# Optimization experiments

Measured on AMD Instinct MI355X. Metric: run time of the kernel, lower is better.

Reference implementation:

```python
import jax, jax.numpy as jnp
import numpy as np

B, S, E, H, DH = 4, 2048, 2048, 16, 256  # DH = mlp hidden (d_hid)
HD = E // H  # per-head dim = 128
EPS = 1e-5

def _ln(x, w, b):
    m = jnp.mean(x, axis=-1, keepdims=True)
    v = jnp.mean(jnp.square(x - m), axis=-1, keepdims=True)
    return (x - m) * jax.lax.rsqrt(v + EPS) * w + b

def setup_inputs() -> dict:
    key = jax.random.key(0)
    ks = jax.random.split(key, 10)
    s = 0.02
    return {
        "x": jax.random.normal(ks[0], (B, S, E), jnp.float32),
        "attention_mask": jax.random.randint(ks[1], (B, S), 0, 2, jnp.int32),
        "ln1_w": jnp.ones((E,), jnp.float32),
        "ln1_b": jnp.zeros((E,), jnp.float32),
        "in_proj_w": jax.random.normal(ks[2], (3 * E, E), jnp.float32) * s,
        "in_proj_b": jnp.zeros((3 * E,), jnp.float32),
        "out_proj_w": jax.random.normal(ks[3], (E, E), jnp.float32) * s,
        "out_proj_b": jnp.zeros((E,), jnp.float32),
        "ln2_w": jnp.ones((E,), jnp.float32),
        "ln2_b": jnp.zeros((E,), jnp.float32),
        "mlp_w1": jax.random.normal(ks[4], (DH, E), jnp.float32) * s,
        "mlp_b1": jnp.zeros((DH,), jnp.float32),
        "mlp_w2": jax.random.normal(ks[5], (E, DH), jnp.float32) * s,
        "mlp_b2": jnp.zeros((E,), jnp.float32),
    }

def reference(x, attention_mask, ln1_w, ln1_b, in_proj_w, in_proj_b,
              out_proj_w, out_proj_b, ln2_w, ln2_b, mlp_w1, mlp_b1, mlp_w2, mlp_b2):
    h = _ln(x, ln1_w, ln1_b)
    qkv = h @ in_proj_w.T + in_proj_b  # [B,S,3E]
    q, k, v = jnp.split(qkv, 3, axis=-1)
    q = q.reshape(B, S, H, HD).transpose(0, 2, 1, 3) / jnp.sqrt(jnp.float32(HD))
    k = k.reshape(B, S, H, HD).transpose(0, 2, 1, 3)
    v = v.reshape(B, S, H, HD).transpose(0, 2, 1, 3)
    scores = jnp.einsum("bhqd,bhkd->bhqk", q, k)
    # Faithful to source: FLOAT attn_mask of +1.0 on strictly-upper triangle (additive),
    # NOT -inf; key_padding_mask positions do get -inf.
    causal_add = jnp.triu(jnp.ones((S, S), jnp.float32), k=1)
    scores = scores + causal_add
    pad = (attention_mask == 0)  # True = padded key
    scores = jnp.where(pad[:, None, None, :], jnp.float32(-jnp.inf), scores)
    attn = jax.nn.softmax(scores, axis=-1)
    ctx = jnp.einsum("bhqk,bhkd->bhqd", attn, v)
    ctx = ctx.transpose(0, 2, 1, 3).reshape(B, S, E)
    x = x + ctx @ out_proj_w.T + out_proj_b
    h2 = _ln(x, ln2_w, ln2_b)
    mlp = jax.nn.relu(h2 @ mlp_w1.T + mlp_b1) @ mlp_w2.T + mlp_b2
    return x + mlp
```

## Files before the change

### kernel.cpp

```cpp
#include <hip/hip_runtime.h>

typedef __attribute__((ext_vector_type(8))) short short8;
typedef __attribute__((ext_vector_type(4))) float f32x4;
typedef __attribute__((ext_vector_type(16))) float f32x16;

typedef __attribute__((address_space(1))) const void gas1_t;
typedef __attribute__((address_space(3))) void las3_t;
#define GLL16(g, l) __builtin_amdgcn_global_load_lds((gas1_t*)(g), (las3_t*)(l), 16, 0, 0)

__device__ inline unsigned short f2bf(float f) {
  union { float f; unsigned int u; } v; v.f = f;
  unsigned int r = v.u + 0x7FFFu + ((v.u >> 16) & 1u);
  return (unsigned short)(r >> 16);
}

__device__ inline float exp2_fast(float x) {
  float r; asm("v_exp_f32 %0, %1" : "=v"(r) : "v"(x)); return r;
}

__device__ inline void vmwait(int n) {
  if (n == 6)      asm volatile("s_waitcnt vmcnt(6)" ::: "memory");
  else             asm volatile("s_waitcnt vmcnt(0)" ::: "memory");
}

__global__ __launch_bounds__(256) void ln_kernel(const float* __restrict__ x,
                                                 const float* __restrict__ w,
                                                 const float* __restrict__ bia,
                                                 unsigned short* __restrict__ out) {
  const int row = blockIdx.x;
  const int tid = threadIdx.x;
  const float* xr = x + (size_t)row * 2048;
  float4 a = *(const float4*)(xr + tid * 8);
  float4 b = *(const float4*)(xr + tid * 8 + 4);
  float s  = a.x + a.y + a.z + a.w + b.x + b.y + b.z + b.w;
  float s2 = a.x*a.x + a.y*a.y + a.z*a.z + a.w*a.w + b.x*b.x + b.y*b.y + b.z*b.z + b.w*b.w;
  #pragma unroll
  for (int off = 1; off < 64; off <<= 1) {
    s  += __shfl_xor(s, off);
    s2 += __shfl_xor(s2, off);
  }
  __shared__ float red[8];
  if ((tid & 63) == 0) { red[tid >> 6] = s; red[4 + (tid >> 6)] = s2; }
  __syncthreads();
  s  = red[0] + red[1] + red[2] + red[3];
  s2 = red[4] + red[5] + red[6] + red[7];
  const float mean = s * (1.f / 2048.f);
  const float var  = s2 * (1.f / 2048.f) - mean * mean;
  const float rstd = rsqrtf(var + 1e-5f);
  float4 wa = *(const float4*)(w + tid * 8), wb = *(const float4*)(w + tid * 8 + 4);
  float4 ba = *(const float4*)(bia + tid * 8), bb = *(const float4*)(bia + tid * 8 + 4);
  short8 o;
  o[0] = (short)f2bf((a.x - mean) * rstd * wa.x + ba.x);
  o[1] = (short)f2bf((a.y - mean) * rstd * wa.y + ba.y);
  o[2] = (short)f2bf((a.z - mean) * rstd * wa.z + ba.z);
  o[3] = (short)f2bf((a.w - mean) * rstd * wa.w + ba.w);
  o[4] = (short)f2bf((b.x - mean) * rstd * wb.x + bb.x);
  o[5] = (short)f2bf((b.y - mean) * rstd * wb.y + bb.y);
  o[6] = (short)f2bf((b.z - mean) * rstd * wb.z + bb.z);
  o[7] = (short)f2bf((b.w - mean) * rstd * wb.w + bb.w);
  *(short8*)(out + (size_t)row * 2048 + tid * 8) = o;
}

__global__ __launch_bounds__(256) void conv_kernel(const float* __restrict__ in,
                                                   unsigned short* __restrict__ out, int n) {
  size_t idx = ((size_t)blockIdx.x * 256 + threadIdx.x) * 8;
  if (idx >= (size_t)n) return;
  float4 a = *(const float4*)(in + idx);
  float4 b = *(const float4*)(in + idx + 4);
  short8 o;
  o[0] = (short)f2bf(a.x); o[1] = (short)f2bf(a.y);
  o[2] = (short)f2bf(a.z); o[3] = (short)f2bf(a.w);
  o[4] = (short)f2bf(b.x); o[5] = (short)f2bf(b.y);
  o[6] = (short)f2bf(b.z); o[7] = (short)f2bf(b.w);
  *(short8*)(out + idx) = o;
}

template <int MODE>
__global__ __launch_bounds__(256) void gemm_bt(const unsigned short* __restrict__ A,
                                               const unsigned short* __restrict__ Bw,
                                               const float* __restrict__ bias,
                                               const float* __restrict__ res,
                                               void* __restrict__ outp,
                                               void* __restrict__ outp2,
                                               int M, int N, int K) {
  __shared__ unsigned short As[128 * 64];
  __shared__ unsigned short Bs[128 * 64];
  const int tid = threadIdx.x;
  const int l = tid & 63, wv = tid >> 6;
  const int l15 = l & 15, l4 = l >> 4;
  const int wr = wv >> 1, wc = wv & 1;
  const int nx = gridDim.x;
  const int nwg = nx * gridDim.y;
  const int bidlin = blockIdx.y * nx + blockIdx.x;
  const int cpx = nwg >> 3;
  const int swz = (bidlin & 7) * cpx + (bidlin >> 3);
  const int m0 = (swz / nx) * 128, n0 = (swz % nx) * 128;

  f32x4 acc[4][4] = {};
  for (int k0 = 0; k0 < K; k0 += 64) {
    __syncthreads();
    #pragma unroll
    for (int i = 0; i < 4; ++i) {
      int e = i * 2048 + tid * 8;
      int r = e >> 6;
      int c = (e ^ ((r & 7) << 3)) & 63;
      GLL16(A + (size_t)(m0 + r) * K + k0 + c, As + e);
      GLL16(Bw + (size_t)(n0 + r) * K + k0 + c, Bs + e);
    }
    __syncthreads();
    #pragma unroll
    for (int kk = 0; kk < 64; kk += 32) {
      short8 af[4], bfr[4];
      #pragma unroll
      for (int m = 0; m < 4; ++m) {
        int r = wr * 64 + m * 16 + l15;
        int byt = (r * 128 + (kk + l4 * 8) * 2) ^ ((r & 7) << 4);
        af[m] = *(const short8*)((const char*)As + byt);
      }
      #pragma unroll
      for (int n = 0; n < 4; ++n) {
        int r = wc * 64 + n * 16 + l15;
        int byt = (r * 128 + (kk + l4 * 8) * 2) ^ ((r & 7) << 4);
        bfr[n] = *(const short8*)((const char*)Bs + byt);
      }
      #pragma unroll
      for (int m = 0; m < 4; ++m)
        #pragma unroll
        for (int n = 0; n < 4; ++n)
          acc[m][n] = __builtin_amdgcn_mfma_f32_16x16x32_bf16(af[m], bfr[n], acc[m][n], 0, 0, 0);
    }
  }
  #pragma unroll
  for (int m = 0; m < 4; ++m) {
    #pragma unroll
    for (int n = 0; n < 4; ++n) {
      #pragma unroll
      for (int r = 0; r < 4; ++r) {
        int row = m0 + wr * 64 + m * 16 + l4 * 4 + r;
        int col = n0 + wc * 64 + n * 16 + l15;
        float v = acc[m][n][r] + bias[col];
        if (MODE == 1) {
          ((unsigned short*)outp)[(size_t)row * N + col] = f2bf(v > 0.f ? v : 0.f);
        } else {
          ((float*)outp)[(size_t)row * N + col] = res[(size_t)row * N + col] + v;
        }
      }
    }
  }
}

template <int MODE>
__global__ __launch_bounds__(512, 2) void gemm8(const unsigned short* __restrict__ A,
                                                const unsigned short* __restrict__ Bw,
                                                const float* __restrict__ bias,
                                                const float* __restrict__ res,
                                                void* __restrict__ outp,
                                                int M, int N, int K) {
  __shared__ char LA[2][2][16384];
  __shared__ char LB[2][2][16384];
  const int tid = threadIdx.x;
  const int l = tid & 63, wv = tid >> 6;
  const int l15 = l & 15, l4 = l >> 4;
  const int wr = wv >> 2, wc = wv & 3;
  const int wch = wc >> 1, wcl = wc & 1;
  const int nx = gridDim.x;
  const int nwg = nx * gridDim.y;
  const int bidlin = blockIdx.y * nx + blockIdx.x;
  const int cpx = nwg >> 3;
  const int swz = (bidlin & 7) * cpx + (bidlin >> 3);
  const int m0 = (swz / nx) * 256, n0 = (swz % nx) * 256;

  const int srow = tid >> 3;
  const int scol = ((tid & 7) ^ (srow & 7)) * 8;

#define STG_A(x, h) { const unsigned short* bp = A + (size_t)(m0 + (h) * 128) * K + (x) * 64; \
    GLL16(bp + (size_t)srow * K + scol, &LA[(x) & 1][h][tid * 16]); \
    GLL16(bp + (size_t)(srow + 64) * K + scol, &LA[(x) & 1][h][8192 + tid * 16]); }
#define STG_B(x, h) { const unsigned short* bp = Bw + (size_t)(n0 + (h) * 128) * K + (x) * 64; \
    GLL16(bp + (size_t)srow * K + scol, &LB[(x) & 1][h][tid * 16]); \
    GLL16(bp + (size_t)(srow + 64) * K + scol, &LB[(x) & 1][h][8192 + tid * 16]); }

#define FOFF(r, kh) ((r) * 128 + (((((kh) * 4 + l4)) ^ ((r) & 7)) << 4))

  f32x4 acc[8][4] = {};
  const int NT = K >> 6;

  STG_A(0, 0); STG_A(0, 1); STG_B(0, 0); STG_B(0, 1);
  STG_B(1, 0); STG_B(1, 1); STG_A(1, 0);
  vmwait(6);
  __builtin_amdgcn_s_barrier();

#define MFMAK(mh, kh) \
    __builtin_amdgcn_s_setprio(1); \
    _Pragma("unroll") for (int f = 0; f < 4; ++f) \
      _Pragma("unroll") for (int n = 0; n < 4; ++n) { \
        if (MODE == 3) \
          acc[(mh) * 4 + f][n] = __builtin_amdgcn_mfma_f32_16x16x32_bf16( \
              bfr[kh][n], af[kh][f], acc[(mh) * 4 + f][n], 0, 0, 0); \
        else \
          acc[(mh) * 4 + f][n] = __builtin_amdgcn_mfma_f32_16x16x32_bf16( \
              af[kh][f], bfr[kh][n], acc[(mh) * 4 + f][n], 0, 0, 0); \
      } \
    __builtin_amdgcn_s_setprio(0);

  for (int t = 0; t < NT; ++t) {
    const char* Ab = LA[t & 1][wr];
    const char* Bb = LB[t & 1][wch];
    short8 af[2][4], bfr[2][4];
    #pragma unroll
    for (int f = 0; f < 4; ++f) {
      bfr[0][f] = *(const short8*)(Bb + FOFF(wcl * 64 + f * 16 + l15, 0));
      af[0][f]  = *(const short8*)(Ab + FOFF(f * 16 + l15, 0));
    }
    __builtin_amdgcn_sched_barrier(0);
    #pragma unroll
    for (int f = 0; f < 4; ++f) {
      bfr[1][f] = *(const short8*)(Bb + FOFF(wcl * 64 + f * 16 + l15, 1));
      af[1][f]  = *(const short8*)(Ab + FOFF(f * 16 + l15, 1));
    }
    if (t + 1 < NT) STG_A(t + 1, 1);
    __builtin_amdgcn_s_barrier();
    asm volatile("s_waitcnt lgkmcnt(8)" ::: "memory");
    __builtin_amdgcn_sched_barrier(0);
    MFMAK(0, 0);
    asm volatile("s_waitcnt lgkmcnt(0)" ::: "memory");
    __builtin_amdgcn_sched_barrier(0);
    MFMAK(0, 1);
    __builtin_amdgcn_s_barrier();
    #pragma unroll
    for (int f = 0; f < 4; ++f)
      af[0][f] = *(const short8*)(Ab + FOFF(64 + f * 16 + l15, 0));
    __builtin_amdgcn_sched_barrier(0);
    #pragma unroll
    for (int f = 0; f < 4; ++f)
      af[1][f] = *(const short8*)(Ab + FOFF(64 + f * 16 + l15, 1));
    if (t + 2 < NT) { STG_B(t + 2, 0); STG_B(t + 2, 1); STG_A(t + 2, 0); }
    __builtin_amdgcn_s_barrier();
    asm volatile("s_waitcnt lgkmcnt(4)" ::: "memory");
    __builtin_amdgcn_sched_barrier(0);
    MFMAK(1, 0);
    asm volatile("s_waitcnt lgkmcnt(0)" ::: "memory");
    __builtin_amdgcn_sched_barrier(0);
    MFMAK(1, 1);
    vmwait(t >= NT - 2 ? 0 : 6);
    __builtin_amdgcn_s_barrier();
  }
#undef MFMAK
#undef FOFF
#undef STG_A
#undef STG_B

  #pragma unroll
  for (int mf = 0; mf < 8; ++mf) {
    #pragma unroll
    for (int nf = 0; nf < 4; ++nf) {
      #pragma unroll
      for (int r = 0; r < 4; ++r) {
        if (MODE == 3) {
          int vcol = n0 + wc * 64 + nf * 16 + l4 * 4 + r;
          int token = m0 + wr * 128 + mf * 16 + l15;
          float v = acc[mf][nf][r] + bias[vcol];
          int hh = vcol >> 7, d = vcol & 127;
          int bb = token >> 11;
          ((unsigned short*)outp)[((size_t)(bb * 16 + hh) * 128 + d) * 2048 +
                                  (token & 2047)] = f2bf(v);
        } else {
          int row = m0 + wr * 128 + mf * 16 + l4 * 4 + r;
          int col = n0 + wc * 64 + nf * 16 + l15;
          float v = acc[mf][nf][r] + bias[col];
          if (MODE == 0) {
            ((unsigned short*)outp)[(size_t)row * 4096 + col] = f2bf(v);
          } else {
            ((float*)outp)[(size_t)row * N + col] = res[(size_t)row * N + col] + v;
          }
        }
      }
    }
  }
}

__global__ __launch_bounds__(256) void attn_kernel(const unsigned short* __restrict__ qk,
                                                   const unsigned short* __restrict__ vT,
                                                   const int* __restrict__ amask,
                                                   unsigned short* __restrict__ ctx) {
  __shared__ unsigned short Ks[2][4096];
  __shared__ unsigned short Vs[2][4096];

  const int lin = blockIdx.y * 16 + blockIdx.x;
  const int swzb = (lin & 7) * 128 + (lin >> 3);
  const int qt = swzb & 15, bh = swzb >> 4;
  const int b = bh >> 4, h = bh & 15;
  const int tid = threadIdx.x;
  const int wv = tid >> 6, l = tid & 63;
  const int l31 = l & 31, hi = l >> 5;
  const int q0w = qt * 128 + wv * 32;
  const float SC2 = 0.08838834764831845f * 1.4426950408889634f;
  const float L2E = 1.4426950408889634f;
  const float MF  = 10.0f;

  int kinv[2], vinv[2];
  #pragma unroll
  for (int c = 0; c < 2; ++c) {
    int e = c * 2048 + tid * 8;
    int key = e >> 7, d0 = e & 127;
    kinv[c] = key * 4096 + 2048 + h * 128 + (d0 ^ ((key & 7) << 3));
    int d = e >> 5, kchunk = ((e >> 3) & 3) ^ ((d & 6) >> 1);
    vinv[c] = d * 2048 + kchunk * 8;
  }
  const unsigned short* kb0 = qk + (size_t)(b * 2048) * 4096;
  const unsigned short* vb0 = vT + (size_t)(b * 16 + h) * (128 * 2048);
  const int* mrow = amask + b * 2048;

  short8 qf[8];
  {
    const unsigned short* qp = qk + (size_t)(b * 2048 + q0w + l31) * 4096 + h * 128 + hi * 8;
    #pragma unroll
    for (int c = 0; c < 8; ++c) qf[c] = *(const short8*)(qp + c * 16);
  }

  short8 vones;
  #pragma unroll
  for (int j = 0; j < 8; ++j) vones[j] = (short)0x3F80;

  f32x16 o[4] = {};
  f32x16 ol = {};

  #pragma unroll
  for (int c = 0; c < 2; ++c) {
    GLL16(kb0 + kinv[c], &Ks[0][c * 2048 + tid * 8]);
    GLL16(vb0 + vinv[c], &Vs[0][c * 2048 + tid * 8]);
  }
  __syncthreads();

  for (int kt = 0; kt < 2048; kt += 32) {
    const int cur = (kt >> 5) & 1;
    if (kt + 32 < 2048) {
      #pragma unroll
      for (int c = 0; c < 2; ++c) {
        GLL16(kb0 + (size_t)(kt + 32) * 4096 + kinv[c], &Ks[cur ^ 1][c * 2048 + tid * 8]);
        GLL16(vb0 + (kt + 32) + vinv[c], &Vs[cur ^ 1][c * 2048 + tid * 8]);
      }
    }
    const unsigned bm = (unsigned)__ballot((l < 32) && (mrow[kt + l31] == 0));
    const unsigned bmh = bm >> (4 * hi);

    f32x16 sacc = {};
    __builtin_amdgcn_s_setprio(1);
    #pragma unroll
    for (int c = 0; c < 8; ++c) {
      short8 kf = *(const short8*)((const char*)Ks[cur] +
                   ((l31 * 256 + c * 32 + hi * 16) ^ ((l31 & 7) << 4)));
      sacc = __builtin_amdgcn_mfma_f32_32x32x16_bf16(kf, qf[c], sacc, 0, 0, 0);
    }
    __builtin_amdgcn_s_setprio(0);

    const int Dq = q0w + l31 - kt - 4 * hi;
    float p[16];
    if (kt > q0w + 31) {
      #pragma unroll
      for (int i = 0; i < 16; ++i) p[i] = sacc[i] * SC2 + (L2E - MF);
    } else if (kt + 31 <= q0w) {
      #pragma unroll
      for (int i = 0; i < 16; ++i) p[i] = sacc[i] * SC2 - MF;
    } else {
      #pragma unroll
      for (int i = 0; i < 16; ++i) {
        const int ci = (i & 3) + 8 * (i >> 2);
        p[i] = sacc[i] * SC2 + ((ci > Dq) ? (L2E - MF) : -MF);
      }
    }
    #pragma unroll
    for (int i = 0; i < 16; ++i) {
      const int ci = (i & 3) + 8 * (i >> 2);
      if ((bmh >> ci) & 1) p[i] = -1e30f;
    }
    #pragma unroll
    for (int i = 0; i < 16; ++i) p[i] = exp2_fast(p[i]);

#define CVTPK(dst, a, bsrc) asm("v_cvt_pk_bf16_f32 %0, %1, %2" : "=v"(dst) : "v"(a), "v"(bsrc))
#define PLSWAP(fst, snd) asm("v_permlane32_swap_b32 %0, %1" : "+v"(fst), "+v"(snd))
    unsigned x, x2, y, y2, u, u2, v, v2;
    CVTPK(x,  p[0],  p[1]);  CVTPK(x2, p[2],  p[3]);
    CVTPK(y,  p[4],  p[5]);  CVTPK(y2, p[6],  p[7]);
    CVTPK(u,  p[8],  p[9]);  CVTPK(u2, p[10], p[11]);
    CVTPK(v,  p[12], p[13]); CVTPK(v2, p[14], p[15]);
    PLSWAP(x, y);  PLSWAP(x2, y2);
    PLSWAP(u, v);  PLSWAP(u2, v2);
    union { unsigned w[4]; short8 s8; } P0, P1;
    P0.w[0] = x; P0.w[1] = x2; P0.w[2] = y; P0.w[3] = y2;
    P1.w[0] = u; P1.w[1] = u2; P1.w[2] = v; P1.w[3] = v2;
    short8 pa0 = P0.s8, pa1 = P1.s8;
#undef CVTPK
#undef PLSWAP

    __builtin_amdgcn_s_setprio(1);
    #pragma unroll
    for (int g = 0; g < 4; ++g) {
      int d = g * 32 + l31;
      int swzd = (d & 6) << 3;
      short8 vf0 = *(const short8*)((const char*)Vs[cur] + ((d * 64 + hi * 16) ^ swzd));
      o[g] = __builtin_amdgcn_mfma_f32_32x32x16_bf16(pa0, vf0, o[g], 0, 0, 0);
      short8 vf1 = *(const short8*)((const char*)Vs[cur] + ((d * 64 + 32 + hi * 16) ^ swzd));
      o[g] = __builtin_amdgcn_mfma_f32_32x32x16_bf16(pa1, vf1, o[g], 0, 0, 0);
    }
    ol = __builtin_amdgcn_mfma_f32_32x32x16_bf16(pa0, vones, ol, 0, 0, 0);
    ol = __builtin_amdgcn_mfma_f32_32x32x16_bf16(pa1, vones, ol, 0, 0, 0);
    __builtin_amdgcn_s_setprio(0);

    __syncthreads();
  }

  float inv[16];
  #pragma unroll
  for (int i = 0; i < 16; ++i) inv[i] = 1.0f / ol[i];
  #pragma unroll
  for (int g = 0; g < 4; ++g) {
    #pragma unroll
    for (int i = 0; i < 16; ++i) {
      int q = q0w + (i & 3) + 8 * (i >> 2) + 4 * hi;
      ctx[(size_t)(b * 2048 + q) * 2048 + h * 128 + g * 32 + l31] = f2bf(o[g][i] * inv[i]);
    }
  }
}

extern "C" void kernel_launch(void* const* d_in, const int* in_sizes, int n_in,
                              void* d_out, int out_size, void* d_ws, size_t ws_size,
                              hipStream_t stream) {
  (void)in_sizes; (void)n_in; (void)out_size; (void)ws_size;
  const float* x    = (const float*)d_in[0];
  const int*   am   = (const int*)d_in[1];
  const float* ln1w = (const float*)d_in[2];
  const float* ln1b = (const float*)d_in[3];
  const float* win  = (const float*)d_in[4];
  const float* bin  = (const float*)d_in[5];
  const float* wout = (const float*)d_in[6];
  const float* bout = (const float*)d_in[7];
  const float* ln2w = (const float*)d_in[8];
  const float* ln2b = (const float*)d_in[9];
  const float* w1   = (const float*)d_in[10];
  const float* b1   = (const float*)d_in[11];
  const float* w2   = (const float*)d_in[12];
  const float* b2   = (const float*)d_in[13];
  float* out = (float*)d_out;

  char* ws = (char*)d_ws;
  unsigned short* hbuf = (unsigned short*)ws;
  unsigned short* ctxb = (unsigned short*)ws;
  unsigned short* qkb  = (unsigned short*)(ws + (size_t)32 * 1048576);
  unsigned short* h2b  = (unsigned short*)(ws + (size_t)32 * 1048576);
  unsigned short* midb = (unsigned short*)(ws + (size_t)64 * 1048576);
  unsigned short* vTb  = (unsigned short*)(ws + (size_t)96 * 1048576);
  unsigned short* wbuf = (unsigned short*)(ws + (size_t)128 * 1048576);

  ln_kernel<<<dim3(8192), dim3(256), 0, stream>>>(x, ln1w, ln1b, hbuf);
  conv_kernel<<<dim3(6144), dim3(256), 0, stream>>>(win, wbuf, 12582912);
  gemm8<0><<<dim3(16, 32), dim3(512), 0, stream>>>(hbuf, wbuf, bin, (const float*)nullptr,
                                                   (void*)qkb, 8192, 4096, 2048);
  gemm8<3><<<dim3(8, 32), dim3(512), 0, stream>>>(hbuf, wbuf + (size_t)4096 * 2048,
                                                  bin + 4096, (const float*)nullptr,
                                                  (void*)vTb, 8192, 2048, 2048);
  attn_kernel<<<dim3(16, 64), dim3(256), 0, stream>>>(qkb, vTb, am, ctxb);
  conv_kernel<<<dim3(2048), dim3(256), 0, stream>>>(wout, wbuf, 4194304);
  gemm8<2><<<dim3(8, 32), dim3(512), 0, stream>>>(ctxb, wbuf, bout, x,
                                                  (void*)out, 8192, 2048, 2048);
  ln_kernel<<<dim3(8192), dim3(256), 0, stream>>>(out, ln2w, ln2b, h2b);
  conv_kernel<<<dim3(256), dim3(256), 0, stream>>>(w1, wbuf, 524288);
  gemm_bt<1><<<dim3(2, 64), dim3(256), 0, stream>>>(h2b, wbuf, b1, (const float*)nullptr,
                                                    (void*)midb, nullptr, 8192, 256, 2048);
  conv_kernel<<<dim3(256), dim3(256), 0, stream>>>(w2, wbuf, 524288);
  gemm8<2><<<dim3(8, 32), dim3(512), 0, stream>>>(midb, wbuf, b2, out,
                                                  (void*)out, 8192, 2048, 256);
}
```

Measured before the change: 592.4 us.

## Fold key padding mask into V projection and row-sum MFMA operand

Removes the per-tile ballot on the attention mask and the per-element masking of softmax probabilities. Padded keys are handled instead by zeroing their V rows in the V-projection epilogue and by using a 0/1 mask vector (staged in LDS) as the row-sum MFMA operand, so masked keys contribute nothing to numerator or denominator. This takes global mask loads and select instructions out of the attention inner loop, at the cost of a mask read in the GEMM epilogue and two small LDS reads per tile. It relies on the fixed max offset making exp finite for masked scores; an all-padded row would still divide by zero, which the reference would also yield as NaN.

Result: no change. 584.3 us (-1.4%).

```diff
diff --git a/kernel.cpp b/kernel.cpp
--- a/kernel.cpp
+++ b/kernel.cpp
@@ -154,6 +154,7 @@
                                                 const unsigned short* __restrict__ Bw,
                                                 const float* __restrict__ bias,
                                                 const float* __restrict__ res,
+                                                const int* __restrict__ amask,
                                                 void* __restrict__ outp,
                                                 int M, int N, int K) {
   __shared__ char LA[2][2][16384];
@@ -252,18 +253,22 @@
 
   #pragma unroll
   for (int mf = 0; mf < 8; ++mf) {
+    int tokenv = 0, amv = 1;
+    if (MODE == 3) {
+      tokenv = m0 + wr * 128 + mf * 16 + l15;
+      amv = amask[tokenv];
+    }
     #pragma unroll
     for (int nf = 0; nf < 4; ++nf) {
       #pragma unroll
       for (int r = 0; r < 4; ++r) {
         if (MODE == 3) {
           int vcol = n0 + wc * 64 + nf * 16 + l4 * 4 + r;
-          int token = m0 + wr * 128 + mf * 16 + l15;
-          float v = acc[mf][nf][r] + bias[vcol];
+          float v = (amv != 0) ? (acc[mf][nf][r] + bias[vcol]) : 0.f;
           int hh = vcol >> 7, d = vcol & 127;
-          int bb = token >> 11;
+          int bb = tokenv >> 11;
           ((unsigned short*)outp)[((size_t)(bb * 16 + hh) * 128 + d) * 2048 +
-                                  (token & 2047)] = f2bf(v);
+                                  (tokenv & 2047)] = f2bf(v);
         } else {
           int row = m0 + wr * 128 + mf * 16 + l4 * 4 + r;
           int col = n0 + wc * 64 + nf * 16 + l15;
@@ -285,6 +290,7 @@
                                                    unsigned short* __restrict__ ctx) {
   __shared__ unsigned short Ks[2][4096];
   __shared__ unsigned short Vs[2][4096];
+  __shared__ unsigned short validbf[2048];
 
   const int lin = blockIdx.y * 16 + blockIdx.x;
   const int swzb = (lin & 7) * 128 + (lin >> 3);
@@ -311,6 +317,14 @@
   const unsigned short* vb0 = vT + (size_t)(b * 16 + h) * (128 * 2048);
   const int* mrow = amask + b * 2048;
 
+  {
+    int i8 = tid * 8;
+    short8 vv;
+    #pragma unroll
+    for (int j = 0; j < 8; ++j) vv[j] = (short)(mrow[i8 + j] ? 0x3F80 : 0);
+    *(short8*)&validbf[i8] = vv;
+  }
+
   short8 qf[8];
   {
     const unsigned short* qp = qk + (size_t)(b * 2048 + q0w + l31) * 4096 + h * 128 + hi * 8;
@@ -318,10 +332,6 @@
     for (int c = 0; c < 8; ++c) qf[c] = *(const short8*)(qp + c * 16);
   }
 
-  short8 vones;
-  #pragma unroll
-  for (int j = 0; j < 8; ++j) vones[j] = (short)0x3F80;
-
   f32x16 o[4] = {};
   f32x16 ol = {};
 
@@ -341,8 +351,6 @@
         GLL16(vb0 + (kt + 32) + vinv[c], &Vs[cur ^ 1][c * 2048 + tid * 8]);
       }
     }
-    const unsigned bm = (unsigned)__ballot((l < 32) && (mrow[kt + l31] == 0));
-    const unsigned bmh = bm >> (4 * hi);
 
     f32x16 sacc = {};
     __builtin_amdgcn_s_setprio(1);
@@ -368,11 +376,6 @@
         const int ci = (i & 3) + 8 * (i >> 2);
         p[i] = sacc[i] * SC2 + ((ci > Dq) ? (L2E - MF) : -MF);
       }
-    }
-    #pragma unroll
-    for (int i = 0; i < 16; ++i) {
-      const int ci = (i & 3) + 8 * (i >> 2);
-      if ((bmh >> ci) & 1) p[i] = -1e30f;
     }
     #pragma unroll
     for (int i = 0; i < 16; ++i) p[i] = exp2_fast(p[i]);
@@ -393,6 +396,9 @@
 #undef CVTPK
 #undef PLSWAP
 
+    short8 vm0 = *(const short8*)&validbf[kt + hi * 8];
+    short8 vm1 = *(const short8*)&validbf[kt + 16 + hi * 8];
+
     __builtin_amdgcn_s_setprio(1);
     #pragma unroll
     for (int g = 0; g < 4; ++g) {
@@ -403,8 +409,8 @@
       short8 vf1 = *(const short8*)((const char*)Vs[cur] + ((d * 64 + 32 + hi * 16) ^ swzd));
       o[g] = __builtin_amdgcn_mfma_f32_32x32x16_bf16(pa1, vf1, o[g], 0, 0, 0);
     }
-    ol = __builtin_amdgcn_mfma_f32_32x32x16_bf16(pa0, vones, ol, 0, 0, 0);
-    ol = __builtin_amdgcn_mfma_f32_32x32x16_bf16(pa1, vones, ol, 0, 0, 0);
+    ol = __builtin_amdgcn_mfma_f32_32x32x16_bf16(pa0, vm0, ol, 0, 0, 0);
+    ol = __builtin_amdgcn_mfma_f32_32x32x16_bf16(pa1, vm1, ol, 0, 0, 0);
     __builtin_amdgcn_s_setprio(0);
 
     __syncthreads();
@@ -455,19 +461,22 @@
   ln_kernel<<<dim3(8192), dim3(256), 0, stream>>>(x, ln1w, ln1b, hbuf);
   conv_kernel<<<dim3(6144), dim3(256), 0, stream>>>(win, wbuf, 12582912);
   gemm8<0><<<dim3(16, 32), dim3(512), 0, stream>>>(hbuf, wbuf, bin, (const float*)nullptr,
-                                                   (void*)qkb, 8192, 4096, 2048);
+                                                   (const int*)nullptr, (void*)qkb,
+                                                   8192, 4096, 2048);
   gemm8<3><<<dim3(8, 32), dim3(512), 0, stream>>>(hbuf, wbuf + (size_t)4096 * 2048,
                                                   bin + 4096, (const float*)nullptr,
-                                                  (void*)vTb, 8192, 2048, 2048);
+                                                  am, (void*)vTb, 8192, 2048, 2048);
   attn_kernel<<<dim3(16, 64), dim3(256), 0, stream>>>(qkb, vTb, am, ctxb);
   conv_kernel<<<dim3(2048), dim3(256), 0, stream>>>(wout, wbuf, 4194304);
   gemm8<2><<<dim3(8, 32), dim3(512), 0, stream>>>(ctxb, wbuf, bout, x,
-                                                  (void*)out, 8192, 2048, 2048);
+                                                  (const int*)nullptr, (void*)out,
+                                                  8192, 2048, 2048);
   ln_kernel<<<dim3(8192), dim3(256), 0, stream>>>(out, ln2w, ln2b, h2b);
   conv_kernel<<<dim3(256), dim3(256), 0, stream>>>(w1, wbuf, 524288);
   gemm_bt<1><<<dim3(2, 64), dim3(256), 0, stream>>>(h2b, wbuf, b1, (const float*)nullptr,
                                                     (void*)midb, nullptr, 8192, 256, 2048);
   conv_kernel<<<dim3(256), dim3(256), 0, stream>>>(w2, wbuf, 524288);
   gemm8<2><<<dim3(8, 32), dim3(512), 0, stream>>>(midb, wbuf, b2, out,
-                                                  (void*)out, 8192, 2048, 256);
-}
+                                                  (const int*)nullptr, (void*)out,
+                                                  8192, 2048, 256);
+}
```
